# Optimization experiments

Measured on AMD Instinct MI355X. Metric: run time of the kernel, lower is better.

Reference implementation:

```python
import jax, jax.numpy as jnp
import numpy as np

N_NODES = 50000
N_EDGES = 1000000
HIDDEN = 64
NUM_GRAPHS = 512
EPS = 1e-5


def _instance_norm(x, seg, num_graphs):
    # per-graph, per-channel normalization (PyG InstanceNorm, affine=False)
    ones = jnp.ones((x.shape[0], 1), x.dtype)
    cnt = jnp.clip(jax.ops.segment_sum(ones, seg, num_segments=num_graphs), 1.0)
    mean = jax.ops.segment_sum(x, seg, num_segments=num_graphs) / cnt
    xc = x - mean[seg]
    var = jax.ops.segment_sum(xc * xc, seg, num_segments=num_graphs) / cnt
    return xc * jax.lax.rsqrt(var + EPS)[seg]


def setup_inputs() -> dict:
    key = jax.random.key(0)
    ks = jax.random.split(key, 10)
    emb = jax.random.normal(ks[0], (N_NODES, HIDDEN), jnp.float32)
    edge_index = jax.random.randint(ks[1], (2, N_EDGES), 0, N_NODES, jnp.int64 if jax.config.read('jax_enable_x64') else jnp.int32)
    batch = jnp.sort(jax.random.randint(ks[2], (N_NODES,), 0, NUM_GRAPHS))
    h = HIDDEN
    # channels = [2h, 4h, h, 1]
    W1 = jax.random.normal(ks[3], (2 * h, 4 * h), jnp.float32) * 0.05
    b1 = jnp.zeros((4 * h,), jnp.float32)
    W2 = jax.random.normal(ks[4], (4 * h, h), jnp.float32) * 0.05
    b2 = jnp.zeros((h,), jnp.float32)
    W3 = jax.random.normal(ks[5], (h, 1), jnp.float32) * 0.05
    b3 = jnp.zeros((1,), jnp.float32)
    return {"emb": emb, "W1": W1, "b1": b1, "W2": W2, "b2": b2,
            "W3": W3, "b3": b3, "edge_index": edge_index, "batch": batch}


def reference(emb, W1, b1, W2, b2, W3, b3, edge_index, batch):
    col, row = edge_index[0], edge_index[1]
    f12 = jnp.concatenate([emb[col], emb[row]], axis=-1)  # [E, 2h]
    seg = batch[col]  # per-edge graph id
    x = f12 @ W1 + b1                                      # [E, 4h]
    x = jax.nn.relu(_instance_norm(x, seg, NUM_GRAPHS))
    x = x @ W2 + b2                                        # [E, h]
    x = jax.nn.relu(_instance_norm(x, seg, NUM_GRAPHS))
    return x @ W3 + b3                                     # [E, 1]
```

## Files before the change

kernel.cpp:

```cpp
#include <hip/hip_runtime.h>
#include <hip/hip_bf16.h>

#define EDGES 1000000
#define NNODES 50000
#define NG 512
#define NTILES 15625
#define NCOLB 50176

typedef __attribute__((ext_vector_type(8))) short bf16x8;
typedef __attribute__((ext_vector_type(4))) float f32x4;

__device__ __forceinline__ unsigned short f2bf(float f){
  unsigned u = __float_as_uint(f);
  u += 0x7fffu + ((u >> 16) & 1u);
  return (unsigned short)(u >> 16);
}
__device__ __forceinline__ float bf2f(unsigned short h){
  return __uint_as_float(((unsigned)h) << 16);
}
__device__ __forceinline__ unsigned pk2bf(float x, float y){
  __hip_bfloat162 h = __float22bfloat162_rn(make_float2(x, y));
  union { __hip_bfloat162 h; unsigned u; } cv; cv.h = h;
  return cv.u;
}
__device__ __forceinline__ int xcd_swizzle(int bid, int nb){
  int nb8 = nb & ~7;
  if (bid >= nb8) return bid;
  int per = nb8 >> 3;
  return (bid & 7) * per + (bid >> 3);
}

__global__ void prep_all(const float* __restrict__ emb, const float* __restrict__ W1,
                         const float* __restrict__ W2,
                         unsigned short* __restrict__ emb_bf,
                         unsigned short* __restrict__ w1tn, unsigned short* __restrict__ w2t){
  int i = blockIdx.x * 256 + threadIdx.x;
  if (i < NNODES * 64){
    emb_bf[i] = f2bf(emb[i]);
  } else {
    int j = i - NNODES * 64;
    if (j < 32768){
      int jj = j >> 6, k = j & 63;
      float v = (jj < 256) ? W1[k * 256 + jj] : W1[(k + 64) * 256 + (jj - 256)];
      w1tn[j] = f2bf(v);
    } else {
      int jj = j - 32768;
      if (jj < 16384){
        int n = jj >> 8, k = jj & 255;
        w2t[jj] = f2bf(W2[k * 64 + n]);
      }
    }
  }
}

__global__ void hists(const int* __restrict__ ei, const int* __restrict__ batch,
                      unsigned* __restrict__ hist, unsigned* __restrict__ chist){
  __shared__ unsigned h[NG];
  int t = threadIdx.x;
  h[t] = 0; h[t + 256] = 0;
  __syncthreads();
  for (int i = 0; i < 4; i++){
    int e = blockIdx.x * 1024 + i * 256 + t;
    if (e < EDGES){
      int cn = ei[e];
      atomicAdd(&chist[cn], 1u);
      atomicAdd(&h[batch[cn]], 1u);
    }
  }
  __syncthreads();
  atomicAdd(&hist[t], h[t]);
  atomicAdd(&hist[t + 256], h[t + 256]);
}

__global__ void col_scan1(const unsigned* __restrict__ chist, unsigned* __restrict__ cpre,
                          unsigned* __restrict__ bsum){
  __shared__ unsigned s[256];
  int t = threadIdx.x;
  int i = blockIdx.x * 256 + t;
  unsigned v = (i < NNODES) ? chist[i] : 0u;
  s[t] = v;
  __syncthreads();
  for (int o = 1; o < 256; o <<= 1){
    unsigned u = (t >= o) ? s[t - o] : 0u;
    __syncthreads();
    s[t] += u;
    __syncthreads();
  }
  cpre[i] = s[t] - v;
  if (t == 255) bsum[blockIdx.x] = s[255];
}

__global__ void col_scan2(unsigned* __restrict__ bsum){
  __shared__ unsigned s[256];
  int t = threadIdx.x;
  unsigned v = (t < 196) ? bsum[t] : 0u;
  s[t] = v;
  __syncthreads();
  for (int o = 1; o < 256; o <<= 1){
    unsigned u = (t >= o) ? s[t - o] : 0u;
    __syncthreads();
    s[t] += u;
    __syncthreads();
  }
  if (t < 196) bsum[t] = s[t] - v;
}

__global__ void col_scan3(unsigned* __restrict__ cpre, const unsigned* __restrict__ bsum){
  int i = blockIdx.x * 256 + threadIdx.x;
  cpre[i] += bsum[blockIdx.x];
}

__global__ void col_scatter(const int* __restrict__ ei, const int* __restrict__ batch,
                            unsigned* __restrict__ cpre, int4* __restrict__ emeta){
  for (int i = 0; i < 4; i++){
    int e = blockIdx.x * 1024 + i * 256 + threadIdx.x;
    if (e < EDGES){
      int cn = ei[e];
      int pos = (int)atomicAdd(&cpre[cn], 1u);
      emeta[pos] = make_int4(cn, ei[EDGES + e], batch[cn], e);
    }
  }
}

__global__ __launch_bounds__(256) void node_gemm(
    const unsigned short* __restrict__ emb_bf, const unsigned short* __restrict__ w1tn,
    unsigned short* __restrict__ P)
{
  __shared__ unsigned short As[64 * 72];
  int t = threadIdx.x;
  int n0 = blockIdx.x * 64;
  {
    int nl = t >> 2, part = t & 3;
    int node = n0 + nl; if (node >= NNODES) node = 0;
    const int4* src = (const int4*)(emb_bf + node * 64 + part * 16);
    int4* dst = (int4*)(As + nl * 72 + part * 16);
    dst[0] = src[0]; dst[1] = src[1];
  }
  __syncthreads();
  int w = t >> 6, lane = t & 63, q = lane >> 4, c = lane & 15;
  f32x4 acc[4][8];
  for (int a = 0; a < 4; a++) for (int b = 0; b < 8; b++) for (int r = 0; r < 4; r++) acc[a][b][r] = 0.f;
  for (int k0 = 0; k0 < 64; k0 += 32){
    bf16x8 af[4];
    for (int tt = 0; tt < 4; tt++) af[tt] = *(const bf16x8*)(As + (tt * 16 + c) * 72 + k0 + q * 8);
    for (int n4 = 0; n4 < 8; n4++){
      bf16x8 bw = *(const bf16x8*)(w1tn + (w * 128 + n4 * 16 + c) * 64 + k0 + q * 8);
      for (int tt = 0; tt < 4; tt++)
        acc[tt][n4] = __builtin_amdgcn_mfma_f32_16x16x32_bf16(af[tt], bw, acc[tt][n4], 0, 0, 0);
    }
  }
  for (int tt = 0; tt < 4; tt++){
    for (int r = 0; r < 4; r++){
      int node = n0 + tt * 16 + q * 4 + r;
      if (node < NNODES){
        unsigned short* dst = P + (size_t)node * 512 + w * 128 + c;
        for (int n4 = 0; n4 < 8; n4++) dst[n4 * 16] = f2bf(acc[tt][n4][r]);
      }
    }
  }
}

__global__ __launch_bounds__(256) void k1_gather(
    const unsigned short* __restrict__ P, const int4* __restrict__ emeta,
    float* __restrict__ sum1, float* __restrict__ sqs1)
{
  int lane = threadIdx.x & 63;
  int bid = xcd_swizzle(blockIdx.x, gridDim.x);
  int wid = (bid * 256 + threadIdx.x) >> 6;
  if (wid >= NTILES) return;
  int p0 = wid * 64;
  int4 me = emeta[p0 + lane];
  int c4 = lane * 4;
  int s0 = __builtin_amdgcn_readlane(me.z, 0);
  bool uni = (__ballot(me.z == s0) == ~0ull);
  float sm0 = 0.f, sm1 = 0.f, sm2 = 0.f, sm3 = 0.f;
  float q0 = 0.f, q1 = 0.f, q2 = 0.f, q3 = 0.f;
  if (uni){
    int cprev = __builtin_amdgcn_readlane(me.x, 0);
    ushort4 a = *(const ushort4*)(P + (size_t)cprev * 512 + c4);
    ushort4 cur[4];
    #pragma unroll
    for (int j = 0; j < 4; j++){
      int re = __builtin_amdgcn_readlane(me.y, j);
      cur[j] = *(const ushort4*)(P + (size_t)re * 512 + 256 + c4);
    }
    for (int eb = 0; eb < 64; eb += 4){
      ushort4 nxt[4];
      if (eb < 60){
        #pragma unroll
        for (int j = 0; j < 4; j++){
          int re = __builtin_amdgcn_readlane(me.y, eb + 4 + j);
          nxt[j] = *(const ushort4*)(P + (size_t)re * 512 + 256 + c4);
        }
      }
      #pragma unroll
      for (int j = 0; j < 4; j++){
        int ce = __builtin_amdgcn_readlane(me.x, eb + j);
        if (ce != cprev){ a = *(const ushort4*)(P + (size_t)ce * 512 + c4); cprev = ce; }
        float x0 = bf2f(a.x) + bf2f(cur[j].x);
        float x1 = bf2f(a.y) + bf2f(cur[j].y);
        float x2v = bf2f(a.z) + bf2f(cur[j].z);
        float x3 = bf2f(a.w) + bf2f(cur[j].w);
        sm0 += x0; q0 += x0 * x0;
        sm1 += x1; q1 += x1 * x1;
        sm2 += x2v; q2 += x2v * x2v;
        sm3 += x3; q3 += x3 * x3;
      }
      #pragma unroll
      for (int j = 0; j < 4; j++) cur[j] = nxt[j];
    }
    float* sp = sum1 + s0 * 256 + c4;
    float* qp = sqs1 + s0 * 256 + c4;
    atomicAdd(sp + 0, sm0); atomicAdd(sp + 1, sm1); atomicAdd(sp + 2, sm2); atomicAdd(sp + 3, sm3);
    atomicAdd(qp + 0, q0);  atomicAdd(qp + 1, q1);  atomicAdd(qp + 2, q2);  atomicAdd(qp + 3, q3);
  } else {
    int cur = s0;
    int cprev = -1;
    ushort4 a = make_ushort4(0,0,0,0);
    for (int e = 0; e < 64; e++){
      int ce = __builtin_amdgcn_readlane(me.x, e);
      int re = __builtin_amdgcn_readlane(me.y, e);
      if (ce != cprev){ a = *(const ushort4*)(P + (size_t)ce * 512 + c4); cprev = ce; }
      ushort4 b = *(const ushort4*)(P + (size_t)re * 512 + 256 + c4);
      int s = __builtin_amdgcn_readlane(me.z, e);
      if (s != cur){
        float* sp = sum1 + cur * 256 + c4;
        float* qp = sqs1 + cur * 256 + c4;
        atomicAdd(sp + 0, sm0); atomicAdd(sp + 1, sm1); atomicAdd(sp + 2, sm2); atomicAdd(sp + 3, sm3);
        atomicAdd(qp + 0, q0);  atomicAdd(qp + 1, q1);  atomicAdd(qp + 2, q2);  atomicAdd(qp + 3, q3);
        sm0 = sm1 = sm2 = sm3 = 0.f; q0 = q1 = q2 = q3 = 0.f;
        cur = s;
      }
      float x0 = bf2f(a.x) + bf2f(b.x);
      float x1 = bf2f(a.y) + bf2f(b.y);
      float x2v = bf2f(a.z) + bf2f(b.z);
      float x3 = bf2f(a.w) + bf2f(b.w);
      sm0 += x0; q0 += x0 * x0;
      sm1 += x1; q1 += x1 * x1;
      sm2 += x2v; q2 += x2v * x2v;
      sm3 += x3; q3 += x3 * x3;
    }
    float* sp = sum1 + cur * 256 + c4;
    float* qp = sqs1 + cur * 256 + c4;
    atomicAdd(sp + 0, sm0); atomicAdd(sp + 1, sm1); atomicAdd(sp + 2, sm2); atomicAdd(sp + 3, sm3);
    atomicAdd(qp + 0, q0);  atomicAdd(qp + 1, q1);  atomicAdd(qp + 2, q2);  atomicAdd(qp + 3, q3);
  }
}

__global__ void finalize1(const float* __restrict__ sum1, const float* __restrict__ sqs1,
                          const unsigned* __restrict__ hist, float* __restrict__ r1,
                          float* __restrict__ mr1){
  int i = blockIdx.x * 256 + threadIdx.x;
  int g = i >> 8;
  float cnt = fmaxf((float)hist[g], 1.f);
  float m = sum1[i] / cnt;
  float v = sqs1[i] / cnt - m * m;
  v = fmaxf(v, 0.f);
  float r = rsqrtf(v + 1e-5f);
  r1[i] = r;
  mr1[i] = m * r;
}

__global__ void finalize2(const float* __restrict__ sum2, const float* __restrict__ sqs2,
                          const unsigned* __restrict__ hist, float* __restrict__ r2,
                          float* __restrict__ mr2){
  int i = blockIdx.x * 256 + threadIdx.x;
  int g = i >> 6;
  float cnt = fmaxf((float)hist[g], 1.f);
  float m = sum2[i] / cnt;
  float v = sqs2[i] / cnt - m * m;
  v = fmaxf(v, 0.f);
  float r = rsqrtf(v + 1e-5f);
  r2[i] = r;
  mr2[i] = m * r;
}

__global__ __launch_bounds__(256) void k2_fused(
    const unsigned short* __restrict__ P, const unsigned short* __restrict__ w2t,
    const int4* __restrict__ emeta,
    const float* __restrict__ r1, const float* __restrict__ mr1,
    float* __restrict__ sum2, float* __restrict__ sqs2,
    unsigned short* __restrict__ x2t)
{
  __shared__ unsigned short Y[64 * 264];
  __shared__ int segl[64];
  __shared__ short rsegA[64];
  __shared__ unsigned char rloA[65];
  __shared__ int nrunS;
  int t = threadIdx.x;
  int bid = xcd_swizzle(blockIdx.x, gridDim.x);
  int p0 = bid * 64;
  int w = t >> 6, lane = t & 63, q = lane >> 4, c = lane & 15;
  int c4 = lane * 4;
  int elb0 = w * 16;
  int4 me = emeta[p0 + elb0 + (lane & 15)];

  ushort4 bb[16];
  #pragma unroll
  for (int e = 0; e < 16; e++){
    int re = __builtin_amdgcn_readlane(me.y, e);
    bb[e] = *(const ushort4*)(P + (size_t)re * 512 + 256 + c4);
  }
  int cprev = __builtin_amdgcn_readlane(me.x, 0);
  ushort4 a = *(const ushort4*)(P + (size_t)cprev * 512 + c4);
  int s0g = __builtin_amdgcn_readlane(me.z, 0);
  float4 r4  = *(const float4*)(r1  + s0g * 256 + c4);
  float4 mr4 = *(const float4*)(mr1 + s0g * 256 + c4);

  if (t < 64) segl[t] = emeta[p0 + t].z;
  if (w == 0){
    int sN = segl[lane];
    int nxt = (lane < 63) ? segl[lane + 1] : sN;
    unsigned long long mask = __ballot(sN != nxt);
    if (lane == 0){
      if (mask == 0ull){
        nrunS = 1; rloA[0] = 0; rloA[1] = 64; rsegA[0] = (short)sN;
      } else {
        int n = 0, cur = segl[0];
        rsegA[0] = (short)cur; rloA[0] = 0;
        for (int i = 1; i < 64; i++)
          if (segl[i] != cur){ cur = segl[i]; n++; rsegA[n] = (short)cur; rloA[n] = (unsigned char)i; }
        rloA[n + 1] = 64; nrunS = n + 1;
      }
    }
  }
  __syncthreads();
  int nrun = nrunS;
  bool uni = (nrun == 1);

  #pragma unroll
  for (int e = 0; e < 16; e++){
    int ce = __builtin_amdgcn_readlane(me.x, e);
    if (ce != cprev){ a = *(const ushort4*)(P + (size_t)ce * 512 + c4); cprev = ce; }
    float4 rr4 = r4, mm4 = mr4;
    if (!uni){
      int s = __builtin_amdgcn_readlane(me.z, e);
      rr4 = *(const float4*)(r1  + s * 256 + c4);
      mm4 = *(const float4*)(mr1 + s * 256 + c4);
    }
    float y0 = fmaxf(0.f, (bf2f(a.x) + bf2f(bb[e].x)) * rr4.x - mm4.x);
    float y1 = fmaxf(0.f, (bf2f(a.y) + bf2f(bb[e].y)) * rr4.y - mm4.y);
    float y2 = fmaxf(0.f, (bf2f(a.z) + bf2f(bb[e].z)) * rr4.z - mm4.z);
    float y3 = fmaxf(0.f, (bf2f(a.w) + bf2f(bb[e].w)) * rr4.w - mm4.w);
    uint2 pk;
    pk.x = pk2bf(y0, y1);
    pk.y = pk2bf(y2, y3);
    *(uint2*)(Y + (elb0 + e) * 264 + c4) = pk;
  }
  __syncthreads();

  f32x4 acc2[4];
  for (int tt = 0; tt < 4; tt++) for (int r = 0; r < 4; r++) acc2[tt][r] = 0.f;
  int ch2 = w * 16 + c;
  for (int kc = 0; kc < 8; kc++){
    int k0 = kc * 32;
    bf16x8 bfr = *(const bf16x8*)(w2t + ch2 * 256 + k0 + q * 8);
    for (int tt = 0; tt < 4; tt++){
      bf16x8 afr = *(const bf16x8*)(Y + (tt * 16 + c) * 264 + k0 + q * 8);
      acc2[tt] = __builtin_amdgcn_mfma_f32_16x16x32_bf16(afr, bfr, acc2[tt], 0, 0, 0);
    }
  }

  if (uni){
    int s = segl[0];
    float sm = 0.f, sq = 0.f;
    for (int tt = 0; tt < 4; tt++)
      for (int r = 0; r < 4; r++){
        float v = acc2[tt][r];
        sm += v; sq += v * v;
      }
    sm += __shfl_xor(sm, 16); sq += __shfl_xor(sq, 16);
    sm += __shfl_xor(sm, 32); sq += __shfl_xor(sq, 32);
    if (q == 0){
      atomicAdd(&sum2[s * 64 + ch2], sm);
      atomicAdd(&sqs2[s * 64 + ch2], sq);
    }
  } else {
    for (int rr = 0; rr < nrun; rr++){
      int s = rsegA[rr], lo = rloA[rr], hi = rloA[rr + 1];
      float sm = 0.f, sq = 0.f;
      for (int tt = 0; tt < 4; tt++){
        int elb = tt * 16 + q * 4;
        for (int r = 0; r < 4; r++){
          int el = elb + r;
          if (el >= lo && el < hi){
            float v = acc2[tt][r];
            sm += v; sq += v * v;
          }
        }
      }
      sm += __shfl_xor(sm, 16); sq += __shfl_xor(sq, 16);
      sm += __shfl_xor(sm, 32); sq += __shfl_xor(sq, 32);
      if (q == 0){
        atomicAdd(&sum2[s * 64 + ch2], sm);
        atomicAdd(&sqs2[s * 64 + ch2], sq);
      }
    }
  }
  for (int tt = 0; tt < 4; tt++){
    uint2 pk;
    pk.x = pk2bf(acc2[tt][0], acc2[tt][1]);
    pk.y = pk2bf(acc2[tt][2], acc2[tt][3]);
    *(uint2*)(x2t + (size_t)ch2 * EDGES + p0 + tt * 16 + q * 4) = pk;
  }
}

__global__ __launch_bounds__(256) void k3_out(
    const unsigned short* __restrict__ x2t, const int4* __restrict__ emeta,
    const float* __restrict__ r2, const float* __restrict__ mr2,
    const float* __restrict__ W3, const float* __restrict__ b3, float* __restrict__ out)
{
  int pp4 = (blockIdx.x * 256 + threadIdx.x) * 4;
  if (pp4 >= EDGES) return;
  int4 m0 = emeta[pp4 + 0];
  int4 m1 = emeta[pp4 + 1];
  int4 m2 = emeta[pp4 + 2];
  int4 m3 = emeta[pp4 + 3];
  float a0 = 0.f, a1 = 0.f, a2 = 0.f, a3 = 0.f;
  if (m0.z == m3.z && m0.z == m1.z && m0.z == m2.z){
    const float* rp = r2  + m0.z * 64;
    const float* mp = mr2 + m0.z * 64;
    #pragma unroll 8
    for (int ch = 0; ch < 64; ch++){
      ushort4 v = *(const ushort4*)(x2t + (size_t)ch * EDGES + pp4);
      float rr = rp[ch], mm = mp[ch], wv = W3[ch];
      a0 += fmaxf(0.f, bf2f(v.x) * rr - mm) * wv;
      a1 += fmaxf(0.f, bf2f(v.y) * rr - mm) * wv;
      a2 += fmaxf(0.f, bf2f(v.z) * rr - mm) * wv;
      a3 += fmaxf(0.f, bf2f(v.w) * rr - mm) * wv;
    }
  } else {
    #pragma unroll 8
    for (int ch = 0; ch < 64; ch++){
      ushort4 v = *(const ushort4*)(x2t + (size_t)ch * EDGES + pp4);
      float wv = W3[ch];
      a0 += fmaxf(0.f, bf2f(v.x) * r2[m0.z * 64 + ch] - mr2[m0.z * 64 + ch]) * wv;
      a1 += fmaxf(0.f, bf2f(v.y) * r2[m1.z * 64 + ch] - mr2[m1.z * 64 + ch]) * wv;
      a2 += fmaxf(0.f, bf2f(v.z) * r2[m2.z * 64 + ch] - mr2[m2.z * 64 + ch]) * wv;
      a3 += fmaxf(0.f, bf2f(v.w) * r2[m3.z * 64 + ch] - mr2[m3.z * 64 + ch]) * wv;
    }
  }
  float bv = b3[0];
  out[m0.w] = a0 + bv;
  out[m1.w] = a1 + bv;
  out[m2.w] = a2 + bv;
  out[m3.w] = a3 + bv;
}

extern "C" void kernel_launch(void* const* d_in, const int* in_sizes, int n_in,
                              void* d_out, int out_size, void* d_ws, size_t ws_size,
                              hipStream_t stream)
{
  (void)in_sizes; (void)n_in; (void)out_size;
  const float* emb = (const float*)d_in[0];
  const float* W1  = (const float*)d_in[1];
  const float* W2  = (const float*)d_in[3];
  const float* W3  = (const float*)d_in[5];
  const float* b3  = (const float*)d_in[6];
  const int* ei    = (const int*)d_in[7];
  const int* batch = (const int*)d_in[8];
  float* out = (float*)d_out;

  char* p = (char*)d_ws;
  size_t off = 0;
  auto take = [&](size_t n) -> char* {
    char* r = p + off;
    off += (n + 255) & ~(size_t)255;
    return r;
  };

  unsigned short* emb_bf = (unsigned short*)take((size_t)NNODES * 64 * 2);
  unsigned short* w1tn   = (unsigned short*)take(32768 * 2);
  unsigned short* w2t    = (unsigned short*)take(16384 * 2);
  int4* emeta = (int4*)take((size_t)EDGES * 16);
  unsigned short* P   = (unsigned short*)take((size_t)NNODES * 512 * 2);
  unsigned short* x2t = (unsigned short*)take((size_t)EDGES * 64 * 2);
  float* r1  = (float*)take(512 * 256 * 4);
  float* mr1 = (float*)take(512 * 256 * 4);
  float* r2  = (float*)take(512 * 64 * 4);
  float* mr2 = (float*)take(512 * 64 * 4);
  unsigned* cpre = (unsigned*)take(NCOLB * 4);
  unsigned* bsum = (unsigned*)take(256 * 4);
  char* zbase = p + off;
  unsigned* hist  = (unsigned*)take(NG * 4);
  unsigned* chist = (unsigned*)take(NCOLB * 4);
  float* sum1 = (float*)take(512 * 256 * 4);
  float* sqs1 = (float*)take(512 * 256 * 4);
  float* sum2 = (float*)take(512 * 64 * 4);
  float* sqs2 = (float*)take(512 * 64 * 4);
  size_t zsize = (size_t)((p + off) - zbase);

  if (ws_size < off) return;

  hipMemsetAsync(zbase, 0, zsize, stream);
  prep_all<<<12692, 256, 0, stream>>>(emb, W1, W2, emb_bf, w1tn, w2t);
  hists<<<977, 256, 0, stream>>>(ei, batch, hist, chist);
  col_scan1<<<196, 256, 0, stream>>>(chist, cpre, bsum);
  col_scan2<<<1, 256, 0, stream>>>(bsum);
  col_scan3<<<196, 256, 0, stream>>>(cpre, bsum);
  col_scatter<<<977, 256, 0, stream>>>(ei, batch, cpre, emeta);
  node_gemm<<<(NNODES + 63) / 64, 256, 0, stream>>>(emb_bf, w1tn, P);
  k1_gather<<<(NTILES + 3) / 4, 256, 0, stream>>>(P, emeta, sum1, sqs1);
  finalize1<<<512, 256, 0, stream>>>(sum1, sqs1, hist, r1, mr1);
  k2_fused<<<NTILES, 256, 0, stream>>>(P, w2t, emeta, r1, mr1, sum2, sqs2, x2t);
  finalize2<<<128, 256, 0, stream>>>(sum2, sqs2, hist, r2, mr2);
  k3_out<<<977, 256, 0, stream>>>(x2t, emeta, r2, mr2, W3, b3, out);
}
```

Before: 575.6 us.

## Materialize layer-1 activations in gather pass, stream them in k2; fuse prep/scan

k1_gather now writes the summed layer-1 pre-norm activations (bf16, E×256) to a workspace buffer when the workspace is large enough. A new k2_stream kernel then reads them contiguously instead of re-gathering rows of P by node index. The emb-to-bf16 conversion moves into node_gemm, and the three-kernel column scan becomes a single 1024-thread kernel. This trades a 512 MB write plus a read for the random gathers of the second pass, and it depends on the harness workspace size to take the new path.

```diff
diff --git a/kernel.cpp b/kernel.cpp
--- a/kernel.cpp
+++ b/kernel.cpp
@@ -30,25 +30,18 @@
   return (bid & 7) * per + (bid >> 3);
 }
 
-__global__ void prep_all(const float* __restrict__ emb, const float* __restrict__ W1,
-                         const float* __restrict__ W2,
-                         unsigned short* __restrict__ emb_bf,
-                         unsigned short* __restrict__ w1tn, unsigned short* __restrict__ w2t){
-  int i = blockIdx.x * 256 + threadIdx.x;
-  if (i < NNODES * 64){
-    emb_bf[i] = f2bf(emb[i]);
+__global__ void prep_w(const float* __restrict__ W1, const float* __restrict__ W2,
+                       unsigned short* __restrict__ w1tn, unsigned short* __restrict__ w2t){
+  int j = blockIdx.x * 256 + threadIdx.x;
+  if (j < 32768){
+    int jj = j >> 6, k = j & 63;
+    float v = (jj < 256) ? W1[k * 256 + jj] : W1[(k + 64) * 256 + (jj - 256)];
+    w1tn[j] = f2bf(v);
   } else {
-    int j = i - NNODES * 64;
-    if (j < 32768){
-      int jj = j >> 6, k = j & 63;
-      float v = (jj < 256) ? W1[k * 256 + jj] : W1[(k + 64) * 256 + (jj - 256)];
-      w1tn[j] = f2bf(v);
-    } else {
-      int jj = j - 32768;
-      if (jj < 16384){
-        int n = jj >> 8, k = jj & 255;
-        w2t[jj] = f2bf(W2[k * 64 + n]);
-      }
+    int i = j - 32768;
+    if (i < 16384){
+      int n = i >> 8, k = i & 255;
+      w2t[i] = f2bf(W2[k * 64 + n]);
     }
   }
 }
@@ -72,42 +65,27 @@
   atomicAdd(&hist[t + 256], h[t + 256]);
 }
 
-__global__ void col_scan1(const unsigned* __restrict__ chist, unsigned* __restrict__ cpre,
-                          unsigned* __restrict__ bsum){
-  __shared__ unsigned s[256];
+__global__ __launch_bounds__(1024) void scan_one(const unsigned* __restrict__ chist,
+                                                 unsigned* __restrict__ cpre){
+  __shared__ unsigned s[1024];
   int t = threadIdx.x;
-  int i = blockIdx.x * 256 + t;
-  unsigned v = (i < NNODES) ? chist[i] : 0u;
-  s[t] = v;
-  __syncthreads();
-  for (int o = 1; o < 256; o <<= 1){
+  int base = t * 49;
+  unsigned sum = 0;
+  for (int i = 0; i < 49; i++) sum += chist[base + i];
+  s[t] = sum;
+  __syncthreads();
+  for (int o = 1; o < 1024; o <<= 1){
     unsigned u = (t >= o) ? s[t - o] : 0u;
     __syncthreads();
     s[t] += u;
     __syncthreads();
   }
-  cpre[i] = s[t] - v;
-  if (t == 255) bsum[blockIdx.x] = s[255];
-}
-
-__global__ void col_scan2(unsigned* __restrict__ bsum){
-  __shared__ unsigned s[256];
-  int t = threadIdx.x;
-  unsigned v = (t < 196) ? bsum[t] : 0u;
-  s[t] = v;
-  __syncthreads();
-  for (int o = 1; o < 256; o <<= 1){
-    unsigned u = (t >= o) ? s[t - o] : 0u;
-    __syncthreads();
-    s[t] += u;
-    __syncthreads();
-  }
-  if (t < 196) bsum[t] = s[t] - v;
-}
-
-__global__ void col_scan3(unsigned* __restrict__ cpre, const unsigned* __restrict__ bsum){
-  int i = blockIdx.x * 256 + threadIdx.x;
-  cpre[i] += bsum[blockIdx.x];
+  unsigned run = s[t] - sum;
+  for (int i = 0; i < 49; i++){
+    unsigned v = chist[base + i];
+    cpre[base + i] = run;
+    run += v;
+  }
 }
 
 __global__ void col_scatter(const int* __restrict__ ei, const int* __restrict__ batch,
@@ -123,7 +101,7 @@
 }
 
 __global__ __launch_bounds__(256) void node_gemm(
-    const unsigned short* __restrict__ emb_bf, const unsigned short* __restrict__ w1tn,
+    const float* __restrict__ emb, const unsigned short* __restrict__ w1tn,
     unsigned short* __restrict__ P)
 {
   __shared__ unsigned short As[64 * 72];
@@ -132,9 +110,11 @@
   {
     int nl = t >> 2, part = t & 3;
     int node = n0 + nl; if (node >= NNODES) node = 0;
-    const int4* src = (const int4*)(emb_bf + node * 64 + part * 16);
-    int4* dst = (int4*)(As + nl * 72 + part * 16);
-    dst[0] = src[0]; dst[1] = src[1];
+    const float4* src = (const float4*)(emb + node * 64 + part * 16);
+    float4 f0 = src[0], f1 = src[1], f2 = src[2], f3 = src[3];
+    uint4* dst = (uint4*)(As + nl * 72 + part * 16);
+    dst[0] = make_uint4(pk2bf(f0.x, f0.y), pk2bf(f0.z, f0.w), pk2bf(f1.x, f1.y), pk2bf(f1.z, f1.w));
+    dst[1] = make_uint4(pk2bf(f2.x, f2.y), pk2bf(f2.z, f2.w), pk2bf(f3.x, f3.y), pk2bf(f3.z, f3.w));
   }
   __syncthreads();
   int w = t >> 6, lane = t & 63, q = lane >> 4, c = lane & 15;
@@ -160,9 +140,10 @@
   }
 }
 
-__global__ __launch_bounds__(256) void k1_gather(
+template<bool STORE>
+__global__ __launch_bounds__(256) void k1_gather_t(
     const unsigned short* __restrict__ P, const int4* __restrict__ emeta,
-    float* __restrict__ sum1, float* __restrict__ sqs1)
+    float* __restrict__ sum1, float* __restrict__ sqs1, unsigned short* __restrict__ x1s)
 {
   int lane = threadIdx.x & 63;
   int bid = xcd_swizzle(blockIdx.x, gridDim.x);
@@ -205,6 +186,12 @@
         sm1 += x1; q1 += x1 * x1;
         sm2 += x2v; q2 += x2v * x2v;
         sm3 += x3; q3 += x3 * x3;
+        if (STORE){
+          uint2 pk;
+          pk.x = pk2bf(x0, x1);
+          pk.y = pk2bf(x2v, x3);
+          *(uint2*)(x1s + (size_t)(p0 + eb + j) * 256 + c4) = pk;
+        }
       }
       #pragma unroll
       for (int j = 0; j < 4; j++) cur[j] = nxt[j];
@@ -239,6 +226,12 @@
       sm1 += x1; q1 += x1 * x1;
       sm2 += x2v; q2 += x2v * x2v;
       sm3 += x3; q3 += x3 * x3;
+      if (STORE){
+        uint2 pk;
+        pk.x = pk2bf(x0, x1);
+        pk.y = pk2bf(x2v, x3);
+        *(uint2*)(x1s + (size_t)(p0 + e) * 256 + c4) = pk;
+      }
     }
     float* sp = sum1 + cur * 256 + c4;
     float* qp = sqs1 + cur * 256 + c4;
@@ -275,8 +268,70 @@
   mr2[i] = m * r;
 }
 
-__global__ __launch_bounds__(256) void k2_fused(
-    const unsigned short* __restrict__ P, const unsigned short* __restrict__ w2t,
+__device__ __forceinline__ void k2_tail(
+    const unsigned short* __restrict__ Y, const unsigned short* __restrict__ w2t,
+    const int* __restrict__ segl, const short* __restrict__ rsegA,
+    const unsigned char* __restrict__ rloA, int nrun,
+    float* __restrict__ sum2, float* __restrict__ sqs2, unsigned short* __restrict__ x2t,
+    int p0, int w, int q, int c)
+{
+  f32x4 acc2[4];
+  for (int tt = 0; tt < 4; tt++) for (int r = 0; r < 4; r++) acc2[tt][r] = 0.f;
+  int ch2 = w * 16 + c;
+  for (int kc = 0; kc < 8; kc++){
+    int k0 = kc * 32;
+    bf16x8 bfr = *(const bf16x8*)(w2t + ch2 * 256 + k0 + q * 8);
+    for (int tt = 0; tt < 4; tt++){
+      bf16x8 afr = *(const bf16x8*)(Y + (tt * 16 + c) * 264 + k0 + q * 8);
+      acc2[tt] = __builtin_amdgcn_mfma_f32_16x16x32_bf16(afr, bfr, acc2[tt], 0, 0, 0);
+    }
+  }
+  if (nrun == 1){
+    int s = segl[0];
+    float sm = 0.f, sq = 0.f;
+    for (int tt = 0; tt < 4; tt++)
+      for (int r = 0; r < 4; r++){
+        float v = acc2[tt][r];
+        sm += v; sq += v * v;
+      }
+    sm += __shfl_xor(sm, 16); sq += __shfl_xor(sq, 16);
+    sm += __shfl_xor(sm, 32); sq += __shfl_xor(sq, 32);
+    if (q == 0){
+      atomicAdd(&sum2[s * 64 + ch2], sm);
+      atomicAdd(&sqs2[s * 64 + ch2], sq);
+    }
+  } else {
+    for (int rr = 0; rr < nrun; rr++){
+      int s = rsegA[rr], lo = rloA[rr], hi = rloA[rr + 1];
+      float sm = 0.f, sq = 0.f;
+      for (int tt = 0; tt < 4; tt++){
+        int elb = tt * 16 + q * 4;
+        for (int r = 0; r < 4; r++){
+          int el = elb + r;
+          if (el >= lo && el < hi){
+            float v = acc2[tt][r];
+            sm += v; sq += v * v;
+          }
+        }
+      }
+      sm += __shfl_xor(sm, 16); sq += __shfl_xor(sq, 16);
+      sm += __shfl_xor(sm, 32); sq += __shfl_xor(sq, 32);
+      if (q == 0){
+        atomicAdd(&sum2[s * 64 + ch2], sm);
+        atomicAdd(&sqs2[s * 64 + ch2], sq);
+      }
+    }
+  }
+  for (int tt = 0; tt < 4; tt++){
+    uint2 pk;
+    pk.x = pk2bf(acc2[tt][0], acc2[tt][1]);
+    pk.y = pk2bf(acc2[tt][2], acc2[tt][3]);
+    *(uint2*)(x2t + (size_t)ch2 * EDGES + p0 + tt * 16 + q * 4) = pk;
+  }
+}
+
+__global__ __launch_bounds__(256) void k2_stream(
+    const unsigned short* __restrict__ x1s, const unsigned short* __restrict__ w2t,
     const int4* __restrict__ emeta,
     const float* __restrict__ r1, const float* __restrict__ mr1,
     float* __restrict__ sum2, float* __restrict__ sqs2,
@@ -293,19 +348,11 @@
   int w = t >> 6, lane = t & 63, q = lane >> 4, c = lane & 15;
   int c4 = lane * 4;
   int elb0 = w * 16;
-  int4 me = emeta[p0 + elb0 + (lane & 15)];
-
-  ushort4 bb[16];
+
+  ushort4 xv[16];
   #pragma unroll
-  for (int e = 0; e < 16; e++){
-    int re = __builtin_amdgcn_readlane(me.y, e);
-    bb[e] = *(const ushort4*)(P + (size_t)re * 512 + 256 + c4);
-  }
-  int cprev = __builtin_amdgcn_readlane(me.x, 0);
-  ushort4 a = *(const ushort4*)(P + (size_t)cprev * 512 + c4);
-  int s0g = __builtin_amdgcn_readlane(me.z, 0);
-  float4 r4  = *(const float4*)(r1  + s0g * 256 + c4);
-  float4 mr4 = *(const float4*)(mr1 + s0g * 256 + c4);
+  for (int e = 0; e < 16; e++)
+    xv[e] = *(const ushort4*)(x1s + (size_t)(p0 + elb0 + e) * 256 + c4);
 
   if (t < 64) segl[t] = emeta[p0 + t].z;
   if (w == 0){
@@ -328,6 +375,86 @@
   int nrun = nrunS;
   bool uni = (nrun == 1);
 
+  float4 r4, mr4;
+  if (uni){
+    int s0 = segl[0];
+    r4  = *(const float4*)(r1  + s0 * 256 + c4);
+    mr4 = *(const float4*)(mr1 + s0 * 256 + c4);
+  }
+  #pragma unroll
+  for (int e = 0; e < 16; e++){
+    float4 rr4 = r4, mm4 = mr4;
+    if (!uni){
+      int s = segl[elb0 + e];
+      rr4 = *(const float4*)(r1  + s * 256 + c4);
+      mm4 = *(const float4*)(mr1 + s * 256 + c4);
+    }
+    float y0 = fmaxf(0.f, bf2f(xv[e].x) * rr4.x - mm4.x);
+    float y1 = fmaxf(0.f, bf2f(xv[e].y) * rr4.y - mm4.y);
+    float y2 = fmaxf(0.f, bf2f(xv[e].z) * rr4.z - mm4.z);
+    float y3 = fmaxf(0.f, bf2f(xv[e].w) * rr4.w - mm4.w);
+    uint2 pk;
+    pk.x = pk2bf(y0, y1);
+    pk.y = pk2bf(y2, y3);
+    *(uint2*)(Y + (elb0 + e) * 264 + c4) = pk;
+  }
+  __syncthreads();
+  k2_tail(Y, w2t, segl, rsegA, rloA, nrun, sum2, sqs2, x2t, p0, w, q, c);
+}
+
+__global__ __launch_bounds__(256) void k2_fused(
+    const unsigned short* __restrict__ P, const unsigned short* __restrict__ w2t,
+    const int4* __restrict__ emeta,
+    const float* __restrict__ r1, const float* __restrict__ mr1,
+    float* __restrict__ sum2, float* __restrict__ sqs2,
+    unsigned short* __restrict__ x2t)
+{
+  __shared__ unsigned short Y[64 * 264];
+  __shared__ int segl[64];
+  __shared__ short rsegA[64];
+  __shared__ unsigned char rloA[65];
+  __shared__ int nrunS;
+  int t = threadIdx.x;
+  int bid = xcd_swizzle(blockIdx.x, gridDim.x);
+  int p0 = bid * 64;
+  int w = t >> 6, lane = t & 63, q = lane >> 4, c = lane & 15;
+  int c4 = lane * 4;
+  int elb0 = w * 16;
+  int4 me = emeta[p0 + elb0 + (lane & 15)];
+
+  ushort4 bb[16];
+  #pragma unroll
+  for (int e = 0; e < 16; e++){
+    int re = __builtin_amdgcn_readlane(me.y, e);
+    bb[e] = *(const ushort4*)(P + (size_t)re * 512 + 256 + c4);
+  }
+  int cprev = __builtin_amdgcn_readlane(me.x, 0);
+  ushort4 a = *(const ushort4*)(P + (size_t)cprev * 512 + c4);
+  int s0g = __builtin_amdgcn_readlane(me.z, 0);
+  float4 r4  = *(const float4*)(r1  + s0g * 256 + c4);
+  float4 mr4 = *(const float4*)(mr1 + s0g * 256 + c4);
+
+  if (t < 64) segl[t] = emeta[p0 + t].z;
+  if (w == 0){
+    int sN = segl[lane];
+    int nxt = (lane < 63) ? segl[lane + 1] : sN;
+    unsigned long long mask = __ballot(sN != nxt);
+    if (lane == 0){
+      if (mask == 0ull){
+        nrunS = 1; rloA[0] = 0; rloA[1] = 64; rsegA[0] = (short)sN;
+      } else {
+        int n = 0, cur = segl[0];
+        rsegA[0] = (short)cur; rloA[0] = 0;
+        for (int i = 1; i < 64; i++)
+          if (segl[i] != cur){ cur = segl[i]; n++; rsegA[n] = (short)cur; rloA[n] = (unsigned char)i; }
+        rloA[n + 1] = 64; nrunS = n + 1;
+      }
+    }
+  }
+  __syncthreads();
+  int nrun = nrunS;
+  bool uni = (nrun == 1);
+
   #pragma unroll
   for (int e = 0; e < 16; e++){
     int ce = __builtin_amdgcn_readlane(me.x, e);
@@ -348,61 +475,7 @@
     *(uint2*)(Y + (elb0 + e) * 264 + c4) = pk;
   }
   __syncthreads();
-
-  f32x4 acc2[4];
-  for (int tt = 0; tt < 4; tt++) for (int r = 0; r < 4; r++) acc2[tt][r] = 0.f;
-  int ch2 = w * 16 + c;
-  for (int kc = 0; kc < 8; kc++){
-    int k0 = kc * 32;
-    bf16x8 bfr = *(const bf16x8*)(w2t + ch2 * 256 + k0 + q * 8);
-    for (int tt = 0; tt < 4; tt++){
-      bf16x8 afr = *(const bf16x8*)(Y + (tt * 16 + c) * 264 + k0 + q * 8);
-      acc2[tt] = __builtin_amdgcn_mfma_f32_16x16x32_bf16(afr, bfr, acc2[tt], 0, 0, 0);
-    }
-  }
-
-  if (uni){
-    int s = segl[0];
-    float sm = 0.f, sq = 0.f;
-    for (int tt = 0; tt < 4; tt++)
-      for (int r = 0; r < 4; r++){
-        float v = acc2[tt][r];
-        sm += v; sq += v * v;
-      }
-    sm += __shfl_xor(sm, 16); sq += __shfl_xor(sq, 16);
-    sm += __shfl_xor(sm, 32); sq += __shfl_xor(sq, 32);
-    if (q == 0){
-      atomicAdd(&sum2[s * 64 + ch2], sm);
-      atomicAdd(&sqs2[s * 64 + ch2], sq);
-    }
-  } else {
-    for (int rr = 0; rr < nrun; rr++){
-      int s = rsegA[rr], lo = rloA[rr], hi = rloA[rr + 1];
-      float sm = 0.f, sq = 0.f;
-      for (int tt = 0; tt < 4; tt++){
-        int elb = tt * 16 + q * 4;
-        for (int r = 0; r < 4; r++){
-          int el = elb + r;
-          if (el >= lo && el < hi){
-            float v = acc2[tt][r];
-            sm += v; sq += v * v;
-          }
-        }
-      }
-      sm += __shfl_xor(sm, 16); sq += __shfl_xor(sq, 16);
-      sm += __shfl_xor(sm, 32); sq += __shfl_xor(sq, 32);
-      if (q == 0){
-        atomicAdd(&sum2[s * 64 + ch2], sm);
-        atomicAdd(&sqs2[s * 64 + ch2], sq);
-      }
-    }
-  }
-  for (int tt = 0; tt < 4; tt++){
-    uint2 pk;
-    pk.x = pk2bf(acc2[tt][0], acc2[tt][1]);
-    pk.y = pk2bf(acc2[tt][2], acc2[tt][3]);
-    *(uint2*)(x2t + (size_t)ch2 * EDGES + p0 + tt * 16 + q * 4) = pk;
-  }
+  k2_tail(Y, w2t, segl, rsegA, rloA, nrun, sum2, sqs2, x2t, p0, w, q, c);
 }
 
 __global__ __launch_bounds__(256) void k3_out(
@@ -469,9 +542,8 @@
     return r;
   };
 
-  unsigned short* emb_bf = (unsigned short*)take((size_t)NNODES * 64 * 2);
-  unsigned short* w1tn   = (unsigned short*)take(32768 * 2);
-  unsigned short* w2t    = (unsigned short*)take(16384 * 2);
+  unsigned short* w1tn = (unsigned short*)take(32768 * 2);
+  unsigned short* w2t  = (unsigned short*)take(16384 * 2);
   int4* emeta = (int4*)take((size_t)EDGES * 16);
   unsigned short* P   = (unsigned short*)take((size_t)NNODES * 512 * 2);
   unsigned short* x2t = (unsigned short*)take((size_t)EDGES * 64 * 2);
@@ -480,7 +552,6 @@
   float* r2  = (float*)take(512 * 64 * 4);
   float* mr2 = (float*)take(512 * 64 * 4);
   unsigned* cpre = (unsigned*)take(NCOLB * 4);
-  unsigned* bsum = (unsigned*)take(256 * 4);
   char* zbase = p + off;
   unsigned* hist  = (unsigned*)take(NG * 4);
   unsigned* chist = (unsigned*)take(NCOLB * 4);
@@ -489,20 +560,28 @@
   float* sum2 = (float*)take(512 * 64 * 4);
   float* sqs2 = (float*)take(512 * 64 * 4);
   size_t zsize = (size_t)((p + off) - zbase);
-
-  if (ws_size < off) return;
+  size_t need_base = off;
+  unsigned short* x1s = (unsigned short*)take((size_t)EDGES * 256 * 2);
+  size_t need_big = off;
+
+  if (ws_size < need_base) return;
+  bool big = (ws_size >= need_big);
 
   hipMemsetAsync(zbase, 0, zsize, stream);
-  prep_all<<<12692, 256, 0, stream>>>(emb, W1, W2, emb_bf, w1tn, w2t);
+  prep_w<<<192, 256, 0, stream>>>(W1, W2, w1tn, w2t);
   hists<<<977, 256, 0, stream>>>(ei, batch, hist, chist);
-  col_scan1<<<196, 256, 0, stream>>>(chist, cpre, bsum);
-  col_scan2<<<1, 256, 0, stream>>>(bsum);
-  col_scan3<<<196, 256, 0, stream>>>(cpre, bsum);
+  scan_one<<<1, 1024, 0, stream>>>(chist, cpre);
   col_scatter<<<977, 256, 0, stream>>>(ei, batch, cpre, emeta);
-  node_gemm<<<(NNODES + 63) / 64, 256, 0, stream>>>(emb_bf, w1tn, P);
-  k1_gather<<<(NTILES + 3) / 4, 256, 0, stream>>>(P, emeta, sum1, sqs1);
-  finalize1<<<512, 256, 0, stream>>>(sum1, sqs1, hist, r1, mr1);
-  k2_fused<<<NTILES, 256, 0, stream>>>(P, w2t, emeta, r1, mr1, sum2, sqs2, x2t);
+  node_gemm<<<(NNODES + 63) / 64, 256, 0, stream>>>(emb, w1tn, P);
+  if (big){
+    k1_gather_t<true><<<(NTILES + 3) / 4, 256, 0, stream>>>(P, emeta, sum1, sqs1, x1s);
+    finalize1<<<512, 256, 0, stream>>>(sum1, sqs1, hist, r1, mr1);
+    k2_stream<<<NTILES, 256, 0, stream>>>(x1s, w2t, emeta, r1, mr1, sum2, sqs2, x2t);
+  } else {
+    k1_gather_t<false><<<(NTILES + 3) / 4, 256, 0, stream>>>(P, emeta, sum1, sqs1, nullptr);
+    finalize1<<<512, 256, 0, stream>>>(sum1, sqs1, hist, r1, mr1);
+    k2_fused<<<NTILES, 256, 0, stream>>>(P, w2t, emeta, r1, mr1, sum2, sqs2, x2t);
+  }
   finalize2<<<128, 256, 0, stream>>>(sum2, sqs2, hist, r2, mr2);
   k3_out<<<977, 256, 0, stream>>>(x2t, emeta, r2, mr2, W3, b3, out);
 }
```

Measured after the change: 593.4 us. +3.1%, slower.

## Gather layer-1 statistics from an FP8 copy of node projections and fuse embedding conversion

Applied to the files above, without the earlier changes.

Adds a kernel that converts the bf16 node projection table P into FP8 e4m3, and switches the first-norm statistics gather to read that FP8 table. This halves the bytes fetched per random gather in that stage. It also folds the fp32-to-bf16 embedding conversion into node_gemm's shared-memory load, which removes the separate emb_bf pass, and moves k2's second GEMM into a helper function. The cost is an extra pass over P, plus a loss of precision in the mean and variance statistics from FP8 rounding, while k2 still reads bf16 P.

```diff
diff --git a/kernel.cpp b/kernel.cpp
--- a/kernel.cpp
+++ b/kernel.cpp
@@ -1,5 +1,6 @@
 #include <hip/hip_runtime.h>
 #include <hip/hip_bf16.h>
+#include <hip/hip_fp8.h>
 
 #define EDGES 1000000
 #define NNODES 50000
@@ -9,6 +10,7 @@
 
 typedef __attribute__((ext_vector_type(8))) short bf16x8;
 typedef __attribute__((ext_vector_type(4))) float f32x4;
+typedef __attribute__((ext_vector_type(2))) float f32x2;
 
 __device__ __forceinline__ unsigned short f2bf(float f){
   unsigned u = __float_as_uint(f);
@@ -23,6 +25,36 @@
   union { __hip_bfloat162 h; unsigned u; } cv; cv.h = h;
   return cv.u;
 }
+
+#if defined(__has_builtin)
+#if __has_builtin(__builtin_amdgcn_cvt_pk_f32_fp8) && __has_builtin(__builtin_amdgcn_cvt_pk_fp8_f32)
+#define HAS_HW_FP8 1
+#endif
+#endif
+
+__device__ __forceinline__ void fp8x4_f32(unsigned u, float& x0, float& x1, float& x2, float& x3){
+#ifdef HAS_HW_FP8
+  f32x2 lo = __builtin_amdgcn_cvt_pk_f32_fp8((int)u, false);
+  f32x2 hi = __builtin_amdgcn_cvt_pk_f32_fp8((int)u, true);
+  x0 = lo[0]; x1 = lo[1]; x2 = hi[0]; x3 = hi[1];
+#else
+  __hip_fp8_e4m3 a, b, c, d;
+  a.__x = u & 0xff; b.__x = (u >> 8) & 0xff; c.__x = (u >> 16) & 0xff; d.__x = (u >> 24) & 0xff;
+  x0 = (float)a; x1 = (float)b; x2 = (float)c; x3 = (float)d;
+#endif
+}
+__device__ __forceinline__ unsigned f32_fp8x4(float x0, float x1, float x2, float x3){
+#ifdef HAS_HW_FP8
+  int w = 0;
+  w = __builtin_amdgcn_cvt_pk_fp8_f32(x0, x1, w, false);
+  w = __builtin_amdgcn_cvt_pk_fp8_f32(x2, x3, w, true);
+  return (unsigned)w;
+#else
+  __hip_fp8_e4m3 a(x0), b(x1), c(x2), d(x3);
+  return (unsigned)a.__x | ((unsigned)b.__x << 8) | ((unsigned)c.__x << 16) | ((unsigned)d.__x << 24);
+#endif
+}
+
 __device__ __forceinline__ int xcd_swizzle(int bid, int nb){
   int nb8 = nb & ~7;
   if (bid >= nb8) return bid;
@@ -30,25 +62,18 @@
   return (bid & 7) * per + (bid >> 3);
 }
 
-__global__ void prep_all(const float* __restrict__ emb, const float* __restrict__ W1,
-                         const float* __restrict__ W2,
-                         unsigned short* __restrict__ emb_bf,
-                         unsigned short* __restrict__ w1tn, unsigned short* __restrict__ w2t){
-  int i = blockIdx.x * 256 + threadIdx.x;
-  if (i < NNODES * 64){
-    emb_bf[i] = f2bf(emb[i]);
+__global__ void prep_w(const float* __restrict__ W1, const float* __restrict__ W2,
+                       unsigned short* __restrict__ w1tn, unsigned short* __restrict__ w2t){
+  int j = blockIdx.x * 256 + threadIdx.x;
+  if (j < 32768){
+    int jj = j >> 6, k = j & 63;
+    float v = (jj < 256) ? W1[k * 256 + jj] : W1[(k + 64) * 256 + (jj - 256)];
+    w1tn[j] = f2bf(v);
   } else {
-    int j = i - NNODES * 64;
-    if (j < 32768){
-      int jj = j >> 6, k = j & 63;
-      float v = (jj < 256) ? W1[k * 256 + jj] : W1[(k + 64) * 256 + (jj - 256)];
-      w1tn[j] = f2bf(v);
-    } else {
-      int jj = j - 32768;
-      if (jj < 16384){
-        int n = jj >> 8, k = jj & 255;
-        w2t[jj] = f2bf(W2[k * 64 + n]);
-      }
+    int i = j - 32768;
+    if (i < 16384){
+      int n = i >> 8, k = i & 255;
+      w2t[i] = f2bf(W2[k * 64 + n]);
     }
   }
 }
@@ -123,7 +148,7 @@
 }
 
 __global__ __launch_bounds__(256) void node_gemm(
-    const unsigned short* __restrict__ emb_bf, const unsigned short* __restrict__ w1tn,
+    const float* __restrict__ emb, const unsigned short* __restrict__ w1tn,
     unsigned short* __restrict__ P)
 {
   __shared__ unsigned short As[64 * 72];
@@ -132,9 +157,11 @@
   {
     int nl = t >> 2, part = t & 3;
     int node = n0 + nl; if (node >= NNODES) node = 0;
-    const int4* src = (const int4*)(emb_bf + node * 64 + part * 16);
-    int4* dst = (int4*)(As + nl * 72 + part * 16);
-    dst[0] = src[0]; dst[1] = src[1];
+    const float4* src = (const float4*)(emb + node * 64 + part * 16);
+    float4 f0 = src[0], f1 = src[1], f2 = src[2], f3 = src[3];
+    uint4* dst = (uint4*)(As + nl * 72 + part * 16);
+    dst[0] = make_uint4(pk2bf(f0.x, f0.y), pk2bf(f0.z, f0.w), pk2bf(f1.x, f1.y), pk2bf(f1.z, f1.w));
+    dst[1] = make_uint4(pk2bf(f2.x, f2.y), pk2bf(f2.z, f2.w), pk2bf(f3.x, f3.y), pk2bf(f3.z, f3.w));
   }
   __syncthreads();
   int w = t >> 6, lane = t & 63, q = lane >> 4, c = lane & 15;
@@ -160,8 +187,16 @@
   }
 }
 
+__global__ void conv_p8(const unsigned short* __restrict__ P, unsigned char* __restrict__ P8){
+  int i4 = blockIdx.x * 256 + threadIdx.x;
+  if (i4 >= (NNODES * 512) / 4) return;
+  ushort4 v = *(const ushort4*)(P + (size_t)i4 * 4);
+  unsigned pk = f32_fp8x4(bf2f(v.x), bf2f(v.y), bf2f(v.z), bf2f(v.w));
+  *(unsigned*)(P8 + (size_t)i4 * 4) = pk;
+}
+
 __global__ __launch_bounds__(256) void k1_gather(
-    const unsigned short* __restrict__ P, const int4* __restrict__ emeta,
+    const unsigned char* __restrict__ P8, const int4* __restrict__ emeta,
     float* __restrict__ sum1, float* __restrict__ sqs1)
 {
   int lane = threadIdx.x & 63;
@@ -177,30 +212,33 @@
   float q0 = 0.f, q1 = 0.f, q2 = 0.f, q3 = 0.f;
   if (uni){
     int cprev = __builtin_amdgcn_readlane(me.x, 0);
-    ushort4 a = *(const ushort4*)(P + (size_t)cprev * 512 + c4);
-    ushort4 cur[4];
+    float a0, a1, a2, a3;
+    fp8x4_f32(*(const unsigned*)(P8 + (size_t)cprev * 512 + c4), a0, a1, a2, a3);
+    unsigned cur[4];
     #pragma unroll
     for (int j = 0; j < 4; j++){
       int re = __builtin_amdgcn_readlane(me.y, j);
-      cur[j] = *(const ushort4*)(P + (size_t)re * 512 + 256 + c4);
+      cur[j] = *(const unsigned*)(P8 + (size_t)re * 512 + 256 + c4);
     }
     for (int eb = 0; eb < 64; eb += 4){
-      ushort4 nxt[4];
+      unsigned nxt[4];
       if (eb < 60){
         #pragma unroll
         for (int j = 0; j < 4; j++){
           int re = __builtin_amdgcn_readlane(me.y, eb + 4 + j);
-          nxt[j] = *(const ushort4*)(P + (size_t)re * 512 + 256 + c4);
+          nxt[j] = *(const unsigned*)(P8 + (size_t)re * 512 + 256 + c4);
         }
       }
       #pragma unroll
       for (int j = 0; j < 4; j++){
         int ce = __builtin_amdgcn_readlane(me.x, eb + j);
-        if (ce != cprev){ a = *(const ushort4*)(P + (size_t)ce * 512 + c4); cprev = ce; }
-        float x0 = bf2f(a.x) + bf2f(cur[j].x);
-        float x1 = bf2f(a.y) + bf2f(cur[j].y);
-        float x2v = bf2f(a.z) + bf2f(cur[j].z);
-        float x3 = bf2f(a.w) + bf2f(cur[j].w);
+        if (ce != cprev){
+          fp8x4_f32(*(const unsigned*)(P8 + (size_t)ce * 512 + c4), a0, a1, a2, a3);
+          cprev = ce;
+        }
+        float b0, b1, b2, b3;
+        fp8x4_f32(cur[j], b0, b1, b2, b3);
+        float x0 = a0 + b0, x1 = a1 + b1, x2v = a2 + b2, x3 = a3 + b3;
         sm0 += x0; q0 += x0 * x0;
         sm1 += x1; q1 += x1 * x1;
         sm2 += x2v; q2 += x2v * x2v;
@@ -216,12 +254,16 @@
   } else {
     int cur = s0;
     int cprev = -1;
-    ushort4 a = make_ushort4(0,0,0,0);
+    float a0 = 0.f, a1 = 0.f, a2 = 0.f, a3 = 0.f;
     for (int e = 0; e < 64; e++){
       int ce = __builtin_amdgcn_readlane(me.x, e);
       int re = __builtin_amdgcn_readlane(me.y, e);
-      if (ce != cprev){ a = *(const ushort4*)(P + (size_t)ce * 512 + c4); cprev = ce; }
-      ushort4 b = *(const ushort4*)(P + (size_t)re * 512 + 256 + c4);
+      if (ce != cprev){
+        fp8x4_f32(*(const unsigned*)(P8 + (size_t)ce * 512 + c4), a0, a1, a2, a3);
+        cprev = ce;
+      }
+      float b0, b1, b2, b3;
+      fp8x4_f32(*(const unsigned*)(P8 + (size_t)re * 512 + 256 + c4), b0, b1, b2, b3);
       int s = __builtin_amdgcn_readlane(me.z, e);
       if (s != cur){
         float* sp = sum1 + cur * 256 + c4;
@@ -231,10 +273,7 @@
         sm0 = sm1 = sm2 = sm3 = 0.f; q0 = q1 = q2 = q3 = 0.f;
         cur = s;
       }
-      float x0 = bf2f(a.x) + bf2f(b.x);
-      float x1 = bf2f(a.y) + bf2f(b.y);
-      float x2v = bf2f(a.z) + bf2f(b.z);
-      float x3 = bf2f(a.w) + bf2f(b.w);
+      float x0 = a0 + b0, x1 = a1 + b1, x2v = a2 + b2, x3 = a3 + b3;
       sm0 += x0; q0 += x0 * x0;
       sm1 += x1; q1 += x1 * x1;
       sm2 += x2v; q2 += x2v * x2v;
@@ -273,6 +312,68 @@
   float r = rsqrtf(v + 1e-5f);
   r2[i] = r;
   mr2[i] = m * r;
+}
+
+__device__ __forceinline__ void k2_tail(
+    const unsigned short* __restrict__ Y, const unsigned short* __restrict__ w2t,
+    const int* __restrict__ segl, const short* __restrict__ rsegA,
+    const unsigned char* __restrict__ rloA, int nrun,
+    float* __restrict__ sum2, float* __restrict__ sqs2, unsigned short* __restrict__ x2t,
+    int p0, int w, int q, int c)
+{
+  f32x4 acc2[4];
+  for (int tt = 0; tt < 4; tt++) for (int r = 0; r < 4; r++) acc2[tt][r] = 0.f;
+  int ch2 = w * 16 + c;
+  for (int kc = 0; kc < 8; kc++){
+    int k0 = kc * 32;
+    bf16x8 bfr = *(const bf16x8*)(w2t + ch2 * 256 + k0 + q * 8);
+    for (int tt = 0; tt < 4; tt++){
+      bf16x8 afr = *(const bf16x8*)(Y + (tt * 16 + c) * 264 + k0 + q * 8);
+      acc2[tt] = __builtin_amdgcn_mfma_f32_16x16x32_bf16(afr, bfr, acc2[tt], 0, 0, 0);
+    }
+  }
+  if (nrun == 1){
+    int s = segl[0];
+    float sm = 0.f, sq = 0.f;
+    for (int tt = 0; tt < 4; tt++)
+      for (int r = 0; r < 4; r++){
+        float v = acc2[tt][r];
+        sm += v; sq += v * v;
+      }
+    sm += __shfl_xor(sm, 16); sq += __shfl_xor(sq, 16);
+    sm += __shfl_xor(sm, 32); sq += __shfl_xor(sq, 32);
+    if (q == 0){
+      atomicAdd(&sum2[s * 64 + ch2], sm);
+      atomicAdd(&sqs2[s * 64 + ch2], sq);
+    }
+  } else {
+    for (int rr = 0; rr < nrun; rr++){
+      int s = rsegA[rr], lo = rloA[rr], hi = rloA[rr + 1];
+      float sm = 0.f, sq = 0.f;
+      for (int tt = 0; tt < 4; tt++){
+        int elb = tt * 16 + q * 4;
+        for (int r = 0; r < 4; r++){
+          int el = elb + r;
+          if (el >= lo && el < hi){
+            float v = acc2[tt][r];
+            sm += v; sq += v * v;
+          }
+        }
+      }
+      sm += __shfl_xor(sm, 16); sq += __shfl_xor(sq, 16);
+      sm += __shfl_xor(sm, 32); sq += __shfl_xor(sq, 32);
+      if (q == 0){
+        atomicAdd(&sum2[s * 64 + ch2], sm);
+        atomicAdd(&sqs2[s * 64 + ch2], sq);
+      }
+    }
+  }
+  for (int tt = 0; tt < 4; tt++){
+    uint2 pk;
+    pk.x = pk2bf(acc2[tt][0], acc2[tt][1]);
+    pk.y = pk2bf(acc2[tt][2], acc2[tt][3]);
+    *(uint2*)(x2t + (size_t)ch2 * EDGES + p0 + tt * 16 + q * 4) = pk;
+  }
 }
 
 __global__ __launch_bounds__(256) void k2_fused(
@@ -348,61 +449,7 @@
     *(uint2*)(Y + (elb0 + e) * 264 + c4) = pk;
   }
   __syncthreads();
-
-  f32x4 acc2[4];
-  for (int tt = 0; tt < 4; tt++) for (int r = 0; r < 4; r++) acc2[tt][r] = 0.f;
-  int ch2 = w * 16 + c;
-  for (int kc = 0; kc < 8; kc++){
-    int k0 = kc * 32;
-    bf16x8 bfr = *(const bf16x8*)(w2t + ch2 * 256 + k0 + q * 8);
-    for (int tt = 0; tt < 4; tt++){
-      bf16x8 afr = *(const bf16x8*)(Y + (tt * 16 + c) * 264 + k0 + q * 8);
-      acc2[tt] = __builtin_amdgcn_mfma_f32_16x16x32_bf16(afr, bfr, acc2[tt], 0, 0, 0);
-    }
-  }
-
-  if (uni){
-    int s = segl[0];
-    float sm = 0.f, sq = 0.f;
-    for (int tt = 0; tt < 4; tt++)
-      for (int r = 0; r < 4; r++){
-        float v = acc2[tt][r];
-        sm += v; sq += v * v;
-      }
-    sm += __shfl_xor(sm, 16); sq += __shfl_xor(sq, 16);
-    sm += __shfl_xor(sm, 32); sq += __shfl_xor(sq, 32);
-    if (q == 0){
-      atomicAdd(&sum2[s * 64 + ch2], sm);
-      atomicAdd(&sqs2[s * 64 + ch2], sq);
-    }
-  } else {
-    for (int rr = 0; rr < nrun; rr++){
-      int s = rsegA[rr], lo = rloA[rr], hi = rloA[rr + 1];
-      float sm = 0.f, sq = 0.f;
-      for (int tt = 0; tt < 4; tt++){
-        int elb = tt * 16 + q * 4;
-        for (int r = 0; r < 4; r++){
-          int el = elb + r;
-          if (el >= lo && el < hi){
-            float v = acc2[tt][r];
-            sm += v; sq += v * v;
-          }
-        }
-      }
-      sm += __shfl_xor(sm, 16); sq += __shfl_xor(sq, 16);
-      sm += __shfl_xor(sm, 32); sq += __shfl_xor(sq, 32);
-      if (q == 0){
-        atomicAdd(&sum2[s * 64 + ch2], sm);
-        atomicAdd(&sqs2[s * 64 + ch2], sq);
-      }
-    }
-  }
-  for (int tt = 0; tt < 4; tt++){
-    uint2 pk;
-    pk.x = pk2bf(acc2[tt][0], acc2[tt][1]);
-    pk.y = pk2bf(acc2[tt][2], acc2[tt][3]);
-    *(uint2*)(x2t + (size_t)ch2 * EDGES + p0 + tt * 16 + q * 4) = pk;
-  }
+  k2_tail(Y, w2t, segl, rsegA, rloA, nrun, sum2, sqs2, x2t, p0, w, q, c);
 }
 
 __global__ __launch_bounds__(256) void k3_out(
@@ -469,11 +516,11 @@
     return r;
   };
 
-  unsigned short* emb_bf = (unsigned short*)take((size_t)NNODES * 64 * 2);
-  unsigned short* w1tn   = (unsigned short*)take(32768 * 2);
-  unsigned short* w2t    = (unsigned short*)take(16384 * 2);
+  unsigned short* w1tn = (unsigned short*)take(32768 * 2);
+  unsigned short* w2t  = (unsigned short*)take(16384 * 2);
   int4* emeta = (int4*)take((size_t)EDGES * 16);
   unsigned short* P   = (unsigned short*)take((size_t)NNODES * 512 * 2);
+  unsigned char*  P8  = (unsigned char*)take((size_t)NNODES * 512);
   unsigned short* x2t = (unsigned short*)take((size_t)EDGES * 64 * 2);
   float* r1  = (float*)take(512 * 256 * 4);
   float* mr1 = (float*)take(512 * 256 * 4);
@@ -493,14 +540,15 @@
   if (ws_size < off) return;
 
   hipMemsetAsync(zbase, 0, zsize, stream);
-  prep_all<<<12692, 256, 0, stream>>>(emb, W1, W2, emb_bf, w1tn, w2t);
+  prep_w<<<192, 256, 0, stream>>>(W1, W2, w1tn, w2t);
   hists<<<977, 256, 0, stream>>>(ei, batch, hist, chist);
   col_scan1<<<196, 256, 0, stream>>>(chist, cpre, bsum);
   col_scan2<<<1, 256, 0, stream>>>(bsum);
   col_scan3<<<196, 256, 0, stream>>>(cpre, bsum);
   col_scatter<<<977, 256, 0, stream>>>(ei, batch, cpre, emeta);
-  node_gemm<<<(NNODES + 63) / 64, 256, 0, stream>>>(emb_bf, w1tn, P);
-  k1_gather<<<(NTILES + 3) / 4, 256, 0, stream>>>(P, emeta, sum1, sqs1);
+  node_gemm<<<(NNODES + 63) / 64, 256, 0, stream>>>(emb, w1tn, P);
+  conv_p8<<<(NNODES * 512 / 4 + 255) / 256, 256, 0, stream>>>(P, P8);
+  k1_gather<<<(NTILES + 3) / 4, 256, 0, stream>>>(P8, emeta, sum1, sqs1);
   finalize1<<<512, 256, 0, stream>>>(sum1, sqs1, hist, r1, mr1);
   k2_fused<<<NTILES, 256, 0, stream>>>(P, w2t, emeta, r1, mr1, sum2, sqs2, x2t);
   finalize2<<<128, 256, 0, stream>>>(sum2, sqs2, hist, r2, mr2);
```

Measured after the change: 590.9 us. 1.03x slower.
